# Performance work log

Measured on AMD Instinct MI355X. Metric: run time of the kernel, lower is better.

The kernel has to match this reference:

```python
import jax, jax.numpy as jnp
import numpy as np

N = 4096       # tokens (batch*seq)
D_IN = 768     # pythia-160m d_model
D_SAE = 32768  # SAE latent dim
K = 64         # top-k active latents


def setup_inputs() -> dict:
    key = jax.random.key(0)
    k1, k2, k3, k4, k5 = jax.random.split(key, 5)
    x = jax.random.normal(k1, (N, D_IN), dtype=jnp.float32)
    W_enc = jax.random.normal(k2, (D_IN, D_SAE), dtype=jnp.float32) * 0.02
    b_enc = jax.random.normal(k3, (D_SAE,), dtype=jnp.float32) * 0.01
    W_dec = jax.random.normal(k4, (D_SAE, D_IN), dtype=jnp.float32) * 0.02
    b_dec = jax.random.normal(k5, (D_IN,), dtype=jnp.float32) * 0.01
    return {"x": x, "W_enc": W_enc, "b_enc": b_enc, "W_dec": W_dec, "b_dec": b_dec}


def reference(x, W_enc, b_enc, W_dec, b_dec):
    # sparsify top-k SAE encode: pre-acts on (x - b_dec), relu, top-k
    pre = (x - b_dec) @ W_enc + b_enc          # [N, D_SAE]
    acts = jax.nn.relu(pre)
    top_acts, top_idx = jax.lax.top_k(acts, K)  # [N, K]
    # decode: equivalent to scatter-to-dense z then z @ W_dec, but gathers
    # only the K active decoder rows per token (same math, no wasted FLOPs)
    recon = jnp.einsum('nk,nkd->nd', top_acts, W_dec[top_idx]) + b_dec  # [N, D_IN]
    return recon
```

## Files before the change

kernel.cpp:

```cpp
#include <hip/hip_runtime.h>
#include <stdint.h>
#include <math.h>

#define NTOK 4096
#define DIN  768
#define DSAE 32768
#define TOPK 64
#define CAP  512
#define CAPLOG 9
#define ZCOEF 0.05f
#define BAND 0.008f
#define BANDCAP 65536
#define BMAX 64

#define GBM 128
#define GBN 256
#define GBK 32
#define NT  (DIN / GBK)
#define SLOT 24576
#define SEGC 24

typedef float f32x4 __attribute__((ext_vector_type(4)));
typedef short short8 __attribute__((ext_vector_type(8)));

__device__ __forceinline__ ushort f2bf(float f) {
  uint32_t u = __float_as_uint(f);
  return (ushort)((u + 0x7fffu + ((u >> 16) & 1u)) >> 16);
}
__device__ __forceinline__ int swz(int o) { return o ^ (((o >> 7) & 3) << 4); }

__global__ __launch_bounds__(256) void k_pre(const float* __restrict__ x,
                                             const float* __restrict__ b_dec,
                                             ushort* __restrict__ Ah,
                                             float* __restrict__ tau,
                                             int* __restrict__ cnt,
                                             int* __restrict__ band_cnt,
                                             const float* __restrict__ W,
                                             float* __restrict__ Wt,
                                             ushort* __restrict__ Bth,
                                             int doWt) {
  __shared__ float Lf[128][33];
  __shared__ float red[4];
  const int bid = blockIdx.x;
  const int t = threadIdx.x;

  if (bid < (DIN / 32) * (DSAE / 128)) {
    const int bk = bid % (DIN / 32);
    const int bn = bid / (DIN / 32);
#pragma unroll
    for (int q = 0; q < 4; ++q) {
      const int idx = q * 256 + t;
      const int k = idx >> 5;
      const int n4 = (idx & 31) * 4;
      const float4 w = *(const float4*)(W + (size_t)(bk * 32 + k) * DSAE + (size_t)bn * 128 + n4);
      Lf[n4 + 0][k] = w.x;
      Lf[n4 + 1][k] = w.y;
      Lf[n4 + 2][k] = w.z;
      Lf[n4 + 3][k] = w.w;
    }
    __syncthreads();
#pragma unroll
    for (int q = 0; q < 4; ++q) {
      const int idx = q * 256 + t;
      const int n = idx >> 3;
      const int k4 = (idx & 7) * 4;
      float4 v;
      v.x = Lf[n][k4 + 0]; v.y = Lf[n][k4 + 1]; v.z = Lf[n][k4 + 2]; v.w = Lf[n][k4 + 3];
      const size_t ob = (size_t)(bn * 128 + n) * DIN + bk * 32 + k4;
      if (doWt) *(float4*)(Wt + ob) = v;
      ushort4 hh;
      hh.x = f2bf(v.x); hh.y = f2bf(v.y); hh.z = f2bf(v.z); hh.w = f2bf(v.w);
      *(ushort4*)(Bth + ob) = hh;
    }
  } else {
    const int row = bid - (DIN / 32) * (DSAE / 128);
    float ss = 0.f;
    if (t < 192) {
      const float4 xv = *(const float4*)(x + (size_t)row * DIN + t * 4);
      const float4 bd = *(const float4*)(b_dec + t * 4);
      const float a0 = xv.x - bd.x, a1 = xv.y - bd.y, a2 = xv.z - bd.z, a3 = xv.w - bd.w;
      ushort4 h;
      h.x = f2bf(a0); h.y = f2bf(a1); h.z = f2bf(a2); h.w = f2bf(a3);
      *(ushort4*)(Ah + (size_t)row * DIN + t * 4) = h;
      ss = a0 * a0 + a1 * a1 + a2 * a2 + a3 * a3;
    }
#pragma unroll
    for (int o = 32; o > 0; o >>= 1) ss += __shfl_down(ss, o, 64);
    const int lane = t & 63, wid = t >> 6;
    if (lane == 0) red[wid] = ss;
    __syncthreads();
    if (t == 0) {
      tau[row] = ZCOEF * sqrtf(red[0] + red[1] + red[2] + red[3]);
      cnt[row] = 0;
      if (row == 0) band_cnt[0] = 0;
    }
  }
}

#define GLD(srcp, dstp) __builtin_amdgcn_global_load_lds( \
    (const __attribute__((address_space(1))) void*)(srcp), \
    (__attribute__((address_space(3))) void*)(dstp), 16, 0, 0)

__global__ __launch_bounds__(512, 4) void k_gemm_mfma(const ushort* __restrict__ Ah,
                                                      const ushort* __restrict__ Bth,
                                                      const float* __restrict__ b_enc,
                                                      const float* __restrict__ tau,
                                                      int* __restrict__ cnt,
                                                      float* __restrict__ cand_v,
                                                      int* __restrict__ cand_i) {
  __shared__ __align__(16) char smem[3 * SLOT];

  const int bid = blockIdx.x;
  const int xcd = bid & 7;
  const int i = bid >> 3;
  const int j = i & 15;
  const int st = i >> 4;
  const int bmg = st >> 3;
  const int bng = st & 7;
  const int bm = bmg * 8 + (j >> 1);
  const int bn = xcd * 16 + bng * 2 + (j & 1);

  const int t = threadIdx.x;
  const int lane = t & 63, wid = t >> 6;
  const int wr = wid >> 2, wc = wid & 3;
  const int fr = lane & 15, fg = lane >> 4;

  f32x4 acc[4][4];
#pragma unroll
  for (int m = 0; m < 4; ++m)
#pragma unroll
    for (int n = 0; n < 4; ++n) acc[m][n] = (f32x4)0.f;

  const int oA = t * 16;
  const int LA = swz(oA);
  const int rA = LA >> 6, eA = (LA & 63) >> 1;
  const int oB0 = t * 16, oB1 = (t + 512) * 16;
  const int LB0 = swz(oB0), LB1 = swz(oB1);
  const int rB0 = LB0 >> 6, eB0 = (LB0 & 63) >> 1;
  const int rB1 = LB1 >> 6, eB1 = (LB1 & 63) >> 1;

  const size_t aRow = (size_t)bm * GBM;
  const size_t bRow = (size_t)bn * GBN;

  auto stage = [&](int slot, int kt) {
    const int k0 = kt * GBK;
    char* sA = smem + slot * SLOT;
    char* sB = sA + 8192;
    GLD(Ah + (aRow + rA) * DIN + k0 + eA, sA + oA);
    GLD(Bth + (bRow + rB0) * DIN + k0 + eB0, sB + oB0);
    GLD(Bth + (bRow + rB1) * DIN + k0 + eB1, sB + oB1);
  };

  stage(0, 0);
  stage(1, 1);

  for (int kt = 0; kt < NT; ++kt) {
    if (kt < NT - 1) {
      asm volatile("s_waitcnt vmcnt(3)" ::: "memory");
    } else {
      asm volatile("s_waitcnt vmcnt(0)" ::: "memory");
    }
    __builtin_amdgcn_s_barrier();
    if (kt + 2 < NT) stage((kt + 2) % 3, kt + 2);

    const char* sA = smem + (kt % 3) * SLOT;
    const char* sB = sA + 8192;
    short8 ah[4], bh[4];
#pragma unroll
    for (int m = 0; m < 4; ++m) {
      const int L = ((wr * 64 + m * 16 + fr) << 6) | (fg << 4);
      ah[m] = *(const short8*)(sA + swz(L));
    }
#pragma unroll
    for (int n = 0; n < 4; ++n) {
      const int L = ((wc * 64 + n * 16 + fr) << 6) | (fg << 4);
      bh[n] = *(const short8*)(sB + swz(L));
    }
#pragma unroll
    for (int m = 0; m < 4; ++m)
#pragma unroll
      for (int n = 0; n < 4; ++n)
        acc[m][n] = __builtin_amdgcn_mfma_f32_16x16x32_bf16(ah[m], bh[n], acc[m][n], 0, 0, 0);
  }

  __syncthreads();
  uint2* seg = (uint2*)smem;
  int* lcnt = (int*)(smem + 128 * SEGC * 8);
  if (t < 128) lcnt[t] = 0;
  __syncthreads();

  const int rbase = bm * GBM;
#pragma unroll
  for (int m = 0; m < 4; ++m) {
#pragma unroll
    for (int jj = 0; jj < 4; ++jj) {
      const int row_l = wr * 64 + m * 16 + fg * 4 + jj;
      const float trow = tau[rbase + row_l];
#pragma unroll
      for (int n = 0; n < 4; ++n) {
        const int col = bn * GBN + wc * 64 + n * 16 + fr;
        const float v = acc[m][n][jj] + b_enc[col];
        if (v > trow) {
          const int sl = atomicAdd(&lcnt[row_l], 1);
          if (sl < SEGC) seg[row_l * SEGC + sl] = make_uint2(__float_as_uint(v), (unsigned)col);
        }
      }
    }
  }
  __syncthreads();
  if (t < 128) {
    const int c = min(lcnt[t], SEGC);
    if (c > 0) {
      const int base = atomicAdd(&cnt[rbase + t], c);
      for (int s2 = 0; s2 < c; ++s2) {
        const int pos = base + s2;
        if (pos < CAP) {
          const uint2 e = seg[t * SEGC + s2];
          cand_v[(size_t)(rbase + t) * CAP + pos] = __uint_as_float(e.x);
          cand_i[(size_t)(rbase + t) * CAP + pos] = (int)e.y;
        }
      }
    }
  }
}

__global__ __launch_bounds__(256) void k_selref(const int* __restrict__ cnt,
                                                const float* __restrict__ cand_v,
                                                const int* __restrict__ cand_i,
                                                const float* __restrict__ x,
                                                const float* __restrict__ Wt,
                                                const float* __restrict__ b_enc,
                                                const float* __restrict__ W_dec,
                                                const float* __restrict__ b_dec,
                                                float* __restrict__ out) {
  const int row = blockIdx.x;
  const int tid = threadIdx.x;
  const int lane = tid & 63, wid = tid >> 6;
  const int c = min(cnt[row], CAP);

  __shared__ unsigned su[CAP];
  __shared__ float sv[CAP];
  __shared__ float xr[DIN];
  __shared__ int redI[4];
  __shared__ int woff[4];
  __shared__ int basev;
  __shared__ int nband;
  __shared__ int bandl[BMAX];
  __shared__ float tv[TOPK];
  __shared__ int ti[TOPK];

  const float* cvr = cand_v + (size_t)row * CAP;
  const int* cir = cand_i + (size_t)row * CAP;
  for (int s = tid; s < c; s += 256) {
    const float v = cvr[s];
    sv[s] = v;
    su[s] = __float_as_uint(v);
  }
  xr[tid] = x[(size_t)row * DIN + tid] - b_dec[tid];
  xr[tid + 256] = x[(size_t)row * DIN + tid + 256] - b_dec[tid + 256];
  xr[tid + 512] = x[(size_t)row * DIN + tid + 512] - b_dec[tid + 512];
  if (tid == 0) nband = 0;
  __syncthreads();

  unsigned T = 0u;
  for (int b = 30; b >= 0; --b) {
    const unsigned Tt = T | (1u << b);
    int cg = 0;
    for (int s = tid; s < c; s += 256) cg += (su[s] >= Tt) ? 1 : 0;
#pragma unroll
    for (int o = 32; o > 0; o >>= 1) cg += __shfl_down(cg, o, 64);
    if (lane == 0) redI[wid] = cg;
    __syncthreads();
    const int tot = redI[0] + redI[1] + redI[2] + redI[3];
    if (tot >= TOPK) T = Tt;
    __syncthreads();
  }
  const float Ta = __uint_as_float(T);

  for (int s = tid; s < c; s += 256) {
    const float v = sv[s];
    if (v >= Ta - BAND && v <= Ta + BAND) {
      const int p = atomicAdd(&nband, 1);
      if (p < BMAX) bandl[p] = s;
    }
  }
  __syncthreads();
  const int nb = min(nband, BMAX);

  for (int e = wid; e < nb; e += 4) {
    const int s = bandl[e];
    const int col = cir[s];
    const float* wrow = Wt + (size_t)col * DIN;
    float acc = 0.f;
#pragma unroll
    for (int jj = 0; jj < 3; ++jj) {
      const float4 a = *(const float4*)&xr[lane * 4 + jj * 256];
      const float4 w = *(const float4*)(wrow + lane * 4 + jj * 256);
      acc = fmaf(a.x, w.x, acc);
      acc = fmaf(a.y, w.y, acc);
      acc = fmaf(a.z, w.z, acc);
      acc = fmaf(a.w, w.w, acc);
    }
#pragma unroll
    for (int o = 32; o > 0; o >>= 1) acc += __shfl_down(acc, o, 64);
    if (lane == 0) {
      const float nv = acc + b_enc[col];
      sv[s] = nv;
      su[s] = __float_as_uint(nv);
    }
  }
  __syncthreads();

  T = 0u;
  for (int b = 30; b >= 0; --b) {
    const unsigned Tt = T | (1u << b);
    int cg = 0;
    for (int s = tid; s < c; s += 256) cg += (su[s] >= Tt) ? 1 : 0;
#pragma unroll
    for (int o = 32; o > 0; o >>= 1) cg += __shfl_down(cg, o, 64);
    if (lane == 0) redI[wid] = cg;
    __syncthreads();
    const int tot = redI[0] + redI[1] + redI[2] + redI[3];
    if (tot >= TOPK) T = Tt;
    __syncthreads();
  }

  if (tid == 0) basev = 0;
  __syncthreads();
  for (int s0 = 0; s0 < c; s0 += 256) {
    const int s = s0 + tid;
    const bool take = (s < c) && (su[s] > T);
    const unsigned long long m = __ballot(take);
    const int wsum = __popcll(m);
    const int wpre = __popcll(m & ((1ull << lane) - 1ull));
    if (lane == 0) woff[wid] = wsum;
    __syncthreads();
    int pre = 0;
    for (int w = 0; w < wid; ++w) pre += woff[w];
    const int tot = woff[0] + woff[1] + woff[2] + woff[3];
    if (take) {
      const int p = basev + pre + wpre;
      tv[p] = sv[s];
      ti[p] = cir[s];
    }
    __syncthreads();
    if (tid == 0) basev += tot;
    __syncthreads();
  }
  for (int s0 = 0; s0 < c; s0 += 256) {
    const int s = s0 + tid;
    const bool take = (s < c) && (su[s] == T);
    const unsigned long long m = __ballot(take);
    const int wsum = __popcll(m);
    const int wpre = __popcll(m & ((1ull << lane) - 1ull));
    if (lane == 0) woff[wid] = wsum;
    __syncthreads();
    int pre = 0;
    for (int w = 0; w < wid; ++w) pre += woff[w];
    const int tot = woff[0] + woff[1] + woff[2] + woff[3];
    if (take) {
      const int p = basev + pre + wpre;
      if (p < TOPK) {
        tv[p] = sv[s];
        ti[p] = cir[s];
      }
    }
    __syncthreads();
    if (tid == 0) basev += tot;
    __syncthreads();
  }

  for (int ksz = 2; ksz <= TOPK; ksz <<= 1) {
    for (int js = ksz >> 1; js > 0; js >>= 1) {
      if (tid < TOPK) {
        const int partner = tid ^ js;
        if (partner > tid) {
          const bool up = ((tid & ksz) == 0);
          const int a = ti[tid], b2 = ti[partner];
          if ((a > b2) == up) {
            ti[tid] = b2;
            ti[partner] = a;
            const float fa = tv[tid];
            tv[tid] = tv[partner];
            tv[partner] = fa;
          }
        }
      }
      __syncthreads();
    }
  }

  if (tid < 192) {
    const int d = tid * 4;
    float4 acc = *(const float4*)(b_dec + d);
#pragma unroll 8
    for (int k = 0; k < TOPK; ++k) {
      const float4 w = *(const float4*)(W_dec + (size_t)ti[k] * DIN + d);
      const float vk = tv[k];
      acc.x = fmaf(vk, w.x, acc.x);
      acc.y = fmaf(vk, w.y, acc.y);
      acc.z = fmaf(vk, w.z, acc.z);
      acc.w = fmaf(vk, w.w, acc.w);
    }
    *(float4*)(out + (size_t)row * DIN + d) = acc;
  }
}

__global__ __launch_bounds__(256) void k_band(const int* __restrict__ cnt,
                                              const float* __restrict__ cand_v,
                                              int* __restrict__ band_cnt,
                                              int* __restrict__ band_list) {
  const int row = blockIdx.x;
  const int tid = threadIdx.x;
  const int lane = tid & 63, wid = tid >> 6;
  const int c = min(cnt[row], CAP);
  __shared__ unsigned su[CAP];
  __shared__ int redI[4];
  const float* cvr = cand_v + (size_t)row * CAP;
  for (int s = tid; s < c; s += 256) su[s] = __float_as_uint(cvr[s]);
  __syncthreads();
  unsigned T = 0u;
  for (int b = 30; b >= 0; --b) {
    const unsigned Tt = T | (1u << b);
    int cg = 0;
    for (int s = tid; s < c; s += 256) cg += (su[s] >= Tt) ? 1 : 0;
#pragma unroll
    for (int o = 32; o > 0; o >>= 1) cg += __shfl_down(cg, o, 64);
    if (lane == 0) redI[wid] = cg;
    __syncthreads();
    const int tot = redI[0] + redI[1] + redI[2] + redI[3];
    if (tot >= TOPK) T = Tt;
    __syncthreads();
  }
  const float Tf = __uint_as_float(T);
  for (int s = tid; s < c; s += 256) {
    const float v = __uint_as_float(su[s]);
    if (v >= Tf - BAND && v <= Tf + BAND) {
      const int p = atomicAdd(band_cnt, 1);
      if (p < BANDCAP) band_list[p] = (row << CAPLOG) + s;
    }
  }
}

__global__ __launch_bounds__(256) void k_refine(const int* __restrict__ band_cnt,
                                                const int* __restrict__ band_list,
                                                const float* __restrict__ x,
                                                const float* __restrict__ b_dec,
                                                const float* __restrict__ W_enc,
                                                const float* __restrict__ b_enc,
                                                float* __restrict__ cand_v,
                                                const int* __restrict__ cand_i) {
  const int i = blockIdx.x * 256 + threadIdx.x;
  const int nb = min(band_cnt[0], BANDCAP);
  if (i >= nb) return;
  const int e = band_list[i];
  const int row = e >> CAPLOG;
  const int s = e & (CAP - 1);
  const int col = cand_i[(size_t)row * CAP + s];
  const float* xr = x + (size_t)row * DIN;
  float acc = 0.f;
  for (int k = 0; k < DIN; ++k)
    acc = fmaf(xr[k] - b_dec[k], W_enc[(size_t)k * DSAE + col], acc);
  cand_v[(size_t)row * CAP + s] = acc + b_enc[col];
}

__global__ __launch_bounds__(256) void k_select(const int* __restrict__ cnt,
                                                const float* __restrict__ cand_v,
                                                const int* __restrict__ cand_i,
                                                float* __restrict__ top_v,
                                                int* __restrict__ top_i) {
  const int row = blockIdx.x;
  const int tid = threadIdx.x;
  const int lane = tid & 63, wid = tid >> 6;
  const int c = min(cnt[row], CAP);
  __shared__ unsigned su[CAP];
  __shared__ float sv[CAP];
  __shared__ int redI[4];
  __shared__ int woff[4];
  __shared__ int basev;
  __shared__ float tv[TOPK];
  __shared__ int ti[TOPK];
  const float* cvr = cand_v + (size_t)row * CAP;
  const int* cir = cand_i + (size_t)row * CAP;
  for (int s = tid; s < c; s += 256) {
    const float v = cvr[s];
    sv[s] = v;
    su[s] = __float_as_uint(v);
  }
  __syncthreads();
  unsigned T = 0u;
  for (int b = 30; b >= 0; --b) {
    const unsigned Tt = T | (1u << b);
    int cg = 0;
    for (int s = tid; s < c; s += 256) cg += (su[s] >= Tt) ? 1 : 0;
#pragma unroll
    for (int o = 32; o > 0; o >>= 1) cg += __shfl_down(cg, o, 64);
    if (lane == 0) redI[wid] = cg;
    __syncthreads();
    const int tot = redI[0] + redI[1] + redI[2] + redI[3];
    if (tot >= TOPK) T = Tt;
    __syncthreads();
  }
  if (tid == 0) basev = 0;
  __syncthreads();
  for (int s0 = 0; s0 < c; s0 += 256) {
    const int s = s0 + tid;
    const bool take = (s < c) && (su[s] > T);
    const unsigned long long m = __ballot(take);
    const int wsum = __popcll(m);
    const int wpre = __popcll(m & ((1ull << lane) - 1ull));
    if (lane == 0) woff[wid] = wsum;
    __syncthreads();
    int pre = 0;
    for (int w = 0; w < wid; ++w) pre += woff[w];
    const int tot = woff[0] + woff[1] + woff[2] + woff[3];
    if (take) {
      const int p = basev + pre + wpre;
      tv[p] = sv[s];
      ti[p] = cir[s];
    }
    __syncthreads();
    if (tid == 0) basev += tot;
    __syncthreads();
  }
  for (int s0 = 0; s0 < c; s0 += 256) {
    const int s = s0 + tid;
    const bool take = (s < c) && (su[s] == T);
    const unsigned long long m = __ballot(take);
    const int wsum = __popcll(m);
    const int wpre = __popcll(m & ((1ull << lane) - 1ull));
    if (lane == 0) woff[wid] = wsum;
    __syncthreads();
    int pre = 0;
    for (int w = 0; w < wid; ++w) pre += woff[w];
    const int tot = woff[0] + woff[1] + woff[2] + woff[3];
    if (take) {
      const int p = basev + pre + wpre;
      if (p < TOPK) {
        tv[p] = sv[s];
        ti[p] = cir[s];
      }
    }
    __syncthreads();
    if (tid == 0) basev += tot;
    __syncthreads();
  }
  for (int ksz = 2; ksz <= TOPK; ksz <<= 1) {
    for (int js = ksz >> 1; js > 0; js >>= 1) {
      if (tid < TOPK) {
        const int partner = tid ^ js;
        if (partner > tid) {
          const bool up = ((tid & ksz) == 0);
          const int a = ti[tid], b2 = ti[partner];
          if ((a > b2) == up) {
            ti[tid] = b2;
            ti[partner] = a;
            const float fa = tv[tid];
            tv[tid] = tv[partner];
            tv[partner] = fa;
          }
        }
      }
      __syncthreads();
    }
  }
  if (tid < TOPK) {
    top_v[(size_t)row * TOPK + tid] = tv[tid];
    top_i[(size_t)row * TOPK + tid] = ti[tid];
  }
}

__global__ __launch_bounds__(192) void k_decode(const float* __restrict__ top_v,
                                                const int* __restrict__ top_i,
                                                const float* __restrict__ W_dec,
                                                const float* __restrict__ b_dec,
                                                float* __restrict__ out) {
  const int row = blockIdx.x;
  const int tid = threadIdx.x;
  __shared__ float v[TOPK];
  __shared__ int ix[TOPK];
  if (tid < TOPK) {
    v[tid] = top_v[(size_t)row * TOPK + tid];
    ix[tid] = top_i[(size_t)row * TOPK + tid];
  }
  __syncthreads();
  const int d = tid * 4;
  float4 acc = *(const float4*)(b_dec + d);
#pragma unroll 8
  for (int k = 0; k < TOPK; ++k) {
    const float4 w = *(const float4*)(W_dec + (size_t)ix[k] * DIN + d);
    const float vk = v[k];
    acc.x = fmaf(vk, w.x, acc.x);
    acc.y = fmaf(vk, w.y, acc.y);
    acc.z = fmaf(vk, w.z, acc.z);
    acc.w = fmaf(vk, w.w, acc.w);
  }
  *(float4*)(out + (size_t)row * DIN + d) = acc;
}

extern "C" void kernel_launch(void* const* d_in, const int* in_sizes, int n_in,
                              void* d_out, int out_size, void* d_ws, size_t ws_size,
                              hipStream_t stream) {
  const float* x = (const float*)d_in[0];
  const float* W_enc = (const float*)d_in[1];
  const float* b_enc = (const float*)d_in[2];
  const float* W_dec = (const float*)d_in[3];
  const float* b_dec = (const float*)d_in[4];
  float* out = (float*)d_out;

  char* p = (char*)d_ws;
  auto alloc = [&](size_t bytes) {
    char* r = p;
    p += (bytes + 255) & ~(size_t)255;
    return r;
  };
  float* tau = (float*)alloc((size_t)NTOK * 4);
  int* cnt = (int*)alloc((size_t)NTOK * 4);
  int* band_cnt = (int*)alloc(256);
  int* band_list = (int*)alloc((size_t)BANDCAP * 4);
  float* cand_v = (float*)alloc((size_t)NTOK * CAP * 4);
  int* cand_i = (int*)alloc((size_t)NTOK * CAP * 4);
  float* top_v = (float*)alloc((size_t)NTOK * TOPK * 4);
  int* top_i = (int*)alloc((size_t)NTOK * TOPK * 4);
  ushort* Ah = (ushort*)alloc((size_t)NTOK * DIN * 2);
  ushort* Bth = (ushort*)alloc((size_t)DSAE * DIN * 2);
  float* Wt = (float*)alloc((size_t)DSAE * DIN * 4);
  const bool fastT = ((size_t)(p - (char*)d_ws) <= ws_size);

  const int nconv = (DIN / 32) * (DSAE / 128);
  hipLaunchKernelGGL(k_pre, dim3(nconv + NTOK), dim3(256), 0, stream,
                     x, b_dec, Ah, tau, cnt, band_cnt, W_enc, Wt, Bth, (int)fastT);
  hipLaunchKernelGGL(k_gemm_mfma, dim3((NTOK / GBM) * (DSAE / GBN)), dim3(512), 0, stream,
                     Ah, Bth, b_enc, tau, cnt, cand_v, cand_i);
  if (fastT) {
    hipLaunchKernelGGL(k_selref, dim3(NTOK), dim3(256), 0, stream,
                       cnt, cand_v, cand_i, x, Wt, b_enc, W_dec, b_dec, out);
  } else {
    hipLaunchKernelGGL(k_band, dim3(NTOK), dim3(256), 0, stream, cnt, cand_v, band_cnt, band_list);
    hipLaunchKernelGGL(k_refine, dim3(BANDCAP / 256), dim3(256), 0, stream,
                       band_cnt, band_list, x, b_dec, W_enc, b_enc, cand_v, cand_i);
    hipLaunchKernelGGL(k_select, dim3(NTOK), dim3(256), 0, stream, cnt, cand_v, cand_i, top_v, top_i);
    hipLaunchKernelGGL(k_decode, dim3(NTOK), dim3(192), 0, stream, top_v, top_i, W_dec, b_dec, out);
  }
}
```

Measured before the change: 430.2 us.

## Replace bitwise threshold search with radix-histogram select and drop index sort

Replaces the 31-round bitwise binary search for the k-th largest candidate (two syncthreads per bit) with a 3–4 round radix histogram select using shared-memory atomics and a wave suffix scan. It removes the bitonic sort of the selected indices in both the select-refine and band kernels, since decode order does not matter. The decode loop now runs four independent accumulators to expose more memory-level parallelism. The truncated 3-round first pass gives an approximate threshold, so the band upper bound is widened slightly, and the different accumulation order may change floating-point rounding.

```diff
diff --git a/kernel.cpp b/kernel.cpp
--- a/kernel.cpp
+++ b/kernel.cpp
@@ -241,7 +241,9 @@
   __shared__ unsigned su[CAP];
   __shared__ float sv[CAP];
   __shared__ float xr[DIN];
-  __shared__ int redI[4];
+  __shared__ int hist[256];
+  __shared__ int wtot[4];
+  __shared__ int selD[2];
   __shared__ int woff[4];
   __shared__ int basev;
   __shared__ int nband;
@@ -262,24 +264,50 @@
   if (tid == 0) nband = 0;
   __syncthreads();
 
-  unsigned T = 0u;
-  for (int b = 30; b >= 0; --b) {
-    const unsigned Tt = T | (1u << b);
-    int cg = 0;
-    for (int s = tid; s < c; s += 256) cg += (su[s] >= Tt) ? 1 : 0;
-#pragma unroll
-    for (int o = 32; o > 0; o >>= 1) cg += __shfl_down(cg, o, 64);
-    if (lane == 0) redI[wid] = cg;
-    __syncthreads();
-    const int tot = redI[0] + redI[1] + redI[2] + redI[3];
-    if (tot >= TOPK) T = Tt;
-    __syncthreads();
-  }
-  const float Ta = __uint_as_float(T);
+  auto kth_largest = [&](int rounds) -> unsigned {
+    const int shv[4] = {23, 15, 7, 0};
+    const int wdv[4] = {8, 8, 8, 7};
+    unsigned pre = 0;
+    int k = TOPK;
+    for (int r = 0; r < rounds; ++r) {
+      const int shift = shv[r];
+      const int NB = 1 << wdv[r];
+      hist[tid] = 0;
+      __syncthreads();
+      const unsigned maskA = ~((1u << (shift + wdv[r])) - 1u);
+      for (int s = tid; s < c; s += 256) {
+        const unsigned u = su[s];
+        if ((u & maskA) == pre) atomicAdd(&hist[(u >> shift) & (NB - 1)], 1);
+      }
+      __syncthreads();
+      const int h = (tid < NB) ? hist[tid] : 0;
+      int sfx = h;
+#pragma unroll
+      for (int o = 1; o < 64; o <<= 1) {
+        const int tmp = __shfl_down(sfx, o, 64);
+        if (lane + o < 64) sfx += tmp;
+      }
+      if (lane == 0) wtot[wid] = sfx;
+      __syncthreads();
+      int S = sfx;
+      for (int w = wid + 1; w < (NB >> 6); ++w) S += wtot[w];
+      if (tid < NB && S >= k && (S - h) < k) {
+        selD[0] = tid;
+        selD[1] = k - (S - h);
+      }
+      __syncthreads();
+      pre |= ((unsigned)selD[0]) << shift;
+      k = selD[1];
+      __syncthreads();
+    }
+    return pre;
+  };
+
+  const float Ta = __uint_as_float(kth_largest(3));
 
   for (int s = tid; s < c; s += 256) {
     const float v = sv[s];
-    if (v >= Ta - BAND && v <= Ta + BAND) {
+    if (v >= Ta - BAND && v <= Ta + BAND + 1.0e-4f) {
       const int p = atomicAdd(&nband, 1);
       if (p < BMAX) bandl[p] = s;
     }
@@ -311,19 +339,7 @@
   }
   __syncthreads();
 
-  T = 0u;
-  for (int b = 30; b >= 0; --b) {
-    const unsigned Tt = T | (1u << b);
-    int cg = 0;
-    for (int s = tid; s < c; s += 256) cg += (su[s] >= Tt) ? 1 : 0;
-#pragma unroll
-    for (int o = 32; o > 0; o >>= 1) cg += __shfl_down(cg, o, 64);
-    if (lane == 0) redI[wid] = cg;
-    __syncthreads();
-    const int tot = redI[0] + redI[1] + redI[2] + redI[3];
-    if (tot >= TOPK) T = Tt;
-    __syncthreads();
-  }
+  const unsigned T = kth_largest(4);
 
   if (tid == 0) basev = 0;
   __syncthreads();
@@ -369,39 +385,34 @@
     if (tid == 0) basev += tot;
     __syncthreads();
   }
-
-  for (int ksz = 2; ksz <= TOPK; ksz <<= 1) {
-    for (int js = ksz >> 1; js > 0; js >>= 1) {
-      if (tid < TOPK) {
-        const int partner = tid ^ js;
-        if (partner > tid) {
-          const bool up = ((tid & ksz) == 0);
-          const int a = ti[tid], b2 = ti[partner];
-          if ((a > b2) == up) {
-            ti[tid] = b2;
-            ti[partner] = a;
-            const float fa = tv[tid];
-            tv[tid] = tv[partner];
-            tv[partner] = fa;
-          }
-        }
-      }
-      __syncthreads();
-    }
-  }
+  __syncthreads();
 
   if (tid < 192) {
     const int d = tid * 4;
-    float4 acc = *(const float4*)(b_dec + d);
-#pragma unroll 8
-    for (int k = 0; k < TOPK; ++k) {
-      const float4 w = *(const float4*)(W_dec + (size_t)ti[k] * DIN + d);
-      const float vk = tv[k];
-      acc.x = fmaf(vk, w.x, acc.x);
-      acc.y = fmaf(vk, w.y, acc.y);
-      acc.z = fmaf(vk, w.z, acc.z);
-      acc.w = fmaf(vk, w.w, acc.w);
-    }
+    float4 a0 = {0.f, 0.f, 0.f, 0.f}, a1 = a0, a2 = a0, a3 = a0;
+#pragma unroll 4
+    for (int kk = 0; kk < 16; ++kk) {
+      const float4 w0 = *(const float4*)(W_dec + (size_t)ti[kk * 4 + 0] * DIN + d);
+      const float4 w1 = *(const float4*)(W_dec + (size_t)ti[kk * 4 + 1] * DIN + d);
+      const float4 w2 = *(const float4*)(W_dec + (size_t)ti[kk * 4 + 2] * DIN + d);
+      const float4 w3 = *(const float4*)(W_dec + (size_t)ti[kk * 4 + 3] * DIN + d);
+      const float v0 = tv[kk * 4 + 0], v1 = tv[kk * 4 + 1];
+      const float v2 = tv[kk * 4 + 2], v3 = tv[kk * 4 + 3];
+      a0.x = fmaf(v0, w0.x, a0.x); a0.y = fmaf(v0, w0.y, a0.y);
+      a0.z = fmaf(v0, w0.z, a0.z); a0.w = fmaf(v0, w0.w, a0.w);
+      a1.x = fmaf(v1, w1.x, a1.x); a1.y = fmaf(v1, w1.y, a1.y);
+      a1.z = fmaf(v1, w1.z, a1.z); a1.w = fmaf(v1, w1.w, a1.w);
+      a2.x = fmaf(v2, w2.x, a2.x); a2.y = fmaf(v2, w2.y, a2.y);
+      a2.z = fmaf(v2, w2.z, a2.z); a2.w = fmaf(v2, w2.w, a2.w);
+      a3.x = fmaf(v3, w3.x, a3.x); a3.y = fmaf(v3, w3.y, a3.y);
+      a3.z = fmaf(v3, w3.z, a3.z); a3.w = fmaf(v3, w3.w, a3.w);
+    }
+    const float4 bd = *(const float4*)(b_dec + d);
+    float4 acc;
+    acc.x = bd.x + ((a0.x + a1.x) + (a2.x + a3.x));
+    acc.y = bd.y + ((a0.y + a1.y) + (a2.y + a3.y));
+    acc.z = bd.z + ((a0.z + a1.z) + (a2.z + a3.z));
+    acc.w = bd.w + ((a0.w + a1.w) + (a2.w + a3.w));
     *(float4*)(out + (size_t)row * DIN + d) = acc;
   }
 }
@@ -545,25 +556,6 @@
     if (tid == 0) basev += tot;
     __syncthreads();
   }
-  for (int ksz = 2; ksz <= TOPK; ksz <<= 1) {
-    for (int js = ksz >> 1; js > 0; js >>= 1) {
-      if (tid < TOPK) {
-        const int partner = tid ^ js;
-        if (partner > tid) {
-          const bool up = ((tid & ksz) == 0);
-          const int a = ti[tid], b2 = ti[partner];
-          if ((a > b2) == up) {
-            ti[tid] = b2;
-            ti[partner] = a;
-            const float fa = tv[tid];
-            tv[tid] = tv[partner];
-            tv[partner] = fa;
-          }
-        }
-      }
-      __syncthreads();
-    }
-  }
   if (tid < TOPK) {
     top_v[(size_t)row * TOPK + tid] = tv[tid];
     top_i[(size_t)row * TOPK + tid] = ti[tid];
```

New measurement: 393.0 us, median of 2. 8.7% less time.
